# Optimization experiments

Hardware: AMD Instinct MI355X
Metric: run time of the kernel (lower is better)

## Reference

```python
import jax, jax.numpy as jnp
import numpy as np

N_NODES = 100000
N_EDGES = 3200000
N_GRAPHS = 128
IN_DIM = 4
HID = 64
BN_EPS = 1e-5


def setup_inputs() -> dict:
    key = jax.random.key(0)
    ks = jax.random.split(key, 24)
    x = jax.random.normal(ks[0], (N_NODES, IN_DIM), dtype=jnp.float32)
    edge_index = jax.random.randint(ks[1], (2, N_EDGES), 0, N_NODES, dtype=jnp.int32)
    batch_ids = jnp.sort(jax.random.randint(ks[2], (N_NODES,), 0, N_GRAPHS, dtype=jnp.int32))

    def lin(k, out_d, in_d):
        s = 1.0 / np.sqrt(in_d)
        return jax.random.uniform(k, (out_d, in_d), jnp.float32, -s, s)

    inp = {
        'x': x, 'edge_index': edge_index, 'batch_ids': batch_ids,
        # SAGEConv i: out = lin_l(mean_neighbors) + lin_r(x_self); bias lives in lin_l
        'w1l': lin(ks[3], HID, IN_DIM), 'b1': jnp.zeros((HID,), jnp.float32), 'w1r': lin(ks[4], HID, IN_DIM),
        'bn1_g': jnp.ones((HID,), jnp.float32), 'bn1_b': jnp.zeros((HID,), jnp.float32),
        'w2l': lin(ks[5], HID, HID), 'b2': jnp.zeros((HID,), jnp.float32), 'w2r': lin(ks[6], HID, HID),
        'bn2_g': jnp.ones((HID,), jnp.float32), 'bn2_b': jnp.zeros((HID,), jnp.float32),
        'w3l': lin(ks[7], HID, HID), 'b3': jnp.zeros((HID,), jnp.float32), 'w3r': lin(ks[8], HID, HID),
        'bn3_g': jnp.ones((HID,), jnp.float32), 'bn3_b': jnp.zeros((HID,), jnp.float32),
        'fc1_w': lin(ks[9], 64, HID), 'fc1_b': jnp.zeros((64,), jnp.float32),
        'fc2_w': lin(ks[10], 2, 64), 'fc2_b': jnp.zeros((2,), jnp.float32),
    }
    return inp


def _sage(x, src, dst, deg_inv, wl, bl, wr):
    # mean-aggregate neighbor messages (source -> target), then two small GEMMs
    msum = jax.ops.segment_sum(x[src], dst, num_segments=N_NODES)  # [N, d]
    agg = msum * deg_inv[:, None]
    return agg @ wl.T + bl + x @ wr.T


def _bn(x, g, b):
    # BatchNorm1d in training mode: batch stats over node dim, biased variance
    m = jnp.mean(x, axis=0)
    v = jnp.mean((x - m) ** 2, axis=0)
    return (x - m) * jax.lax.rsqrt(v + BN_EPS) * g + b


def reference(x, edge_index, batch_ids,
              w1l, b1, w1r, bn1_g, bn1_b,
              w2l, b2, w2r, bn2_g, bn2_b,
              w3l, b3, w3r, bn3_g, bn3_b,
              fc1_w, fc1_b, fc2_w, fc2_b):
    src, dst = edge_index[0], edge_index[1]
    deg = jax.ops.segment_sum(jnp.ones((src.shape[0],), x.dtype), dst, num_segments=N_NODES)
    deg_inv = 1.0 / jnp.maximum(deg, 1.0)

    h = jax.nn.relu(_bn(_sage(x, src, dst, deg_inv, w1l, b1, w1r), bn1_g, bn1_b))
    h = jax.nn.relu(_bn(_sage(h, src, dst, deg_inv, w2l, b2, w2r), bn2_g, bn2_b))
    h = jax.nn.relu(_bn(_sage(h, src, dst, deg_inv, w3l, b3, w3r), bn3_g, bn3_b))

    # global_mean_pool over graphs
    gsum = jax.ops.segment_sum(h, batch_ids, num_segments=N_GRAPHS)
    gcnt = jax.ops.segment_sum(jnp.ones((h.shape[0],), h.dtype), batch_ids, num_segments=N_GRAPHS)
    pooled = gsum / jnp.maximum(gcnt, 1.0)[:, None]

    # MLP head (dropout = identity at inference)
    hid = jax.nn.relu(pooled @ fc1_w.T + fc1_b)
    return hid @ fc2_w.T + fc2_b
```

## Files before the change

kernel.cpp:

```cpp
#include <hip/hip_runtime.h>
#include <hip/hip_fp16.h>

#define NN 100000
#define NE 3200000
#define NG 128
#define BN_EPS 1e-5f

#define NBUK 782
#define BSHIFT 7
#define BCAP 6144

#define GRID_SG 1024
#define PBMAX 2048
#define PSLICE 8

typedef _Float16 h2v __attribute__((ext_vector_type(2)));
typedef unsigned int u32x2 __attribute__((ext_vector_type(2)));
typedef unsigned int u32x4 __attribute__((ext_vector_type(4)));

static __device__ __forceinline__ h2v as_h2(unsigned int u) {
    return __builtin_bit_cast(h2v, u);
}
static __device__ __forceinline__ unsigned int as_u32(h2v h) {
    return __builtin_bit_cast(unsigned int, h);
}


__global__ void __launch_bounds__(512) k_scatter(
    const int* __restrict__ src, const int* __restrict__ dst,
    int* __restrict__ slab_cursor, unsigned int* __restrict__ slab, int E) {
    __shared__ int hist[NBUK + 2];
    __shared__ int cbase[NBUK + 2];
    int tid = threadIdx.x;
    int eBeg = blockIdx.x * 12500;
    int eEnd = min(eBeg + 12500, E);

    for (int t = tid; t < NBUK; t += 512) hist[t] = 0;
    __syncthreads();
    for (int e = eBeg + tid; e < eEnd; e += 512) {
        int b = dst[e] >> BSHIFT;
        atomicAdd(&hist[b], 1);
    }
    __syncthreads();
    for (int t = tid; t < NBUK; t += 512) {
        int c = hist[t];
        cbase[t] = (c > 0) ? atomicAdd(&slab_cursor[t], c) : 0;
    }
    __syncthreads();
    for (int t = tid; t < NBUK; t += 512) hist[t] = 0;
    __syncthreads();
    for (int e = eBeg + tid; e < eEnd; e += 512) {
        int d = dst[e];
        int b = d >> BSHIFT;
        int r = atomicAdd(&hist[b], 1);
        int pos = cbase[b] + r;
        if (pos < BCAP) slab[(size_t)b * BCAP + pos] = ((unsigned)src[e] << BSHIFT) | (unsigned)(d & 127);
    }
}

__global__ void __launch_bounds__(512) k_bucket_csr(
    const unsigned int* __restrict__ slab, const int* __restrict__ slab_cursor,
    int* __restrict__ row_ptr,
    float* __restrict__ deg_inv, int* __restrict__ csr_src,
    const float* __restrict__ x, const float* __restrict__ w1l,
    const float* __restrict__ b1, const float* __restrict__ w1r,
    __half* __restrict__ hp16, float* __restrict__ part) {
    __shared__ int lds_csr[BCAP];
    __shared__ int red[512];
    __shared__ int sdeg[128];
    __shared__ int sscan[128];
    __shared__ int slcur[128];
    __shared__ float swl[256], swr[256], sb1[64];
    __shared__ float ssum[64], ssq[64];
    int tid = threadIdx.x;
    int b = blockIdx.x;
    int lo = b << BSHIFT;
    int cnt = min(slab_cursor[b], BCAP);
    const unsigned int* sl = slab + (size_t)b * BCAP;

    int partial = 0;
    for (int j = tid; j < b; j += 512) partial += min(slab_cursor[j], BCAP);
    red[tid] = partial;
    __syncthreads();
    for (int off = 256; off > 0; off >>= 1) {
        if (tid < off) red[tid] += red[tid + off];
        __syncthreads();
    }
    int base = red[0];
    if (b == NBUK - 1 && tid == 0) row_ptr[NN] = base + cnt;

    if (tid < 256) { swl[tid] = w1l[tid]; swr[tid] = w1r[tid]; }
    if (tid < 64)  { sb1[tid] = b1[tid]; ssum[tid] = 0.f; ssq[tid] = 0.f; }
    if (tid < 128) sdeg[tid] = 0;
    __syncthreads();

    unsigned int myv[12];
    int mycount = 0;
    for (int k = tid; k < cnt; k += 512) myv[mycount++] = sl[k];
#pragma unroll
    for (int j = 0; j < 12; j++)
        if (j < mycount) atomicAdd(&sdeg[myv[j] & 127], 1);
    __syncthreads();
    int v = (tid < 128) ? sdeg[tid] : 0;
    if (tid < 128) sscan[tid] = v;
    __syncthreads();
    for (int off = 1; off < 128; off <<= 1) {
        int add = 0;
        if (tid < 128 && tid >= off) add = sscan[tid - off];
        __syncthreads();
        if (tid < 128) sscan[tid] += add;
        __syncthreads();
    }
    if (tid < 128) {
        int excl = sscan[tid] - v;
        int n = lo + tid;
        if (n < NN) {
            row_ptr[n] = base + excl;
            deg_inv[n] = 1.0f / fmaxf((float)v, 1.0f);
        }
        slcur[tid] = excl;
    }
    __syncthreads();
#pragma unroll
    for (int j = 0; j < 12; j++)
        if (j < mycount) {
            unsigned int p = myv[j];
            int pos = atomicAdd(&slcur[p & 127], 1);
            lds_csr[pos] = (int)(p >> BSHIFT);
        }
    __syncthreads();
    for (int k = tid; k < cnt; k += 512) csr_src[base + k] = lds_csr[k];

    int i = tid >> 2, c = tid & 3;
    int n = lo + i;
    bool valid = (n < NN);
    int dhi = sscan[i];
    int dlo = dhi - sdeg[i];
    const float4* x4 = (const float4*)x;
    float4 acc = make_float4(0.f, 0.f, 0.f, 0.f);
    int k = dlo + c;
    for (; k + 12 < dhi; k += 16) {
        int s0 = lds_csr[k], s1 = lds_csr[k + 4], s2 = lds_csr[k + 8], s3 = lds_csr[k + 12];
        float4 v0 = x4[s0];
        float4 v1 = x4[s1];
        float4 v2 = x4[s2];
        float4 v3 = x4[s3];
        acc.x += v0.x + v1.x + v2.x + v3.x;
        acc.y += v0.y + v1.y + v2.y + v3.y;
        acc.z += v0.z + v1.z + v2.z + v3.z;
        acc.w += v0.w + v1.w + v2.w + v3.w;
    }
    for (; k < dhi; k += 4) {
        int s = lds_csr[k];
        float4 xv = x4[s];
        acc.x += xv.x; acc.y += xv.y; acc.z += xv.z; acc.w += xv.w;
    }
#pragma unroll
    for (int m = 1; m <= 2; m <<= 1) {
        acc.x += __shfl_xor(acc.x, m);
        acc.y += __shfl_xor(acc.y, m);
        acc.z += __shfl_xor(acc.z, m);
        acc.w += __shfl_xor(acc.w, m);
    }
    float dv = 1.0f / fmaxf((float)sdeg[i], 1.0f);
    float ax = acc.x * dv, ay = acc.y * dv, az = acc.z * dv, aw = acc.w * dv;
    float4 xs = valid ? x4[n] : make_float4(0.f, 0.f, 0.f, 0.f);

#pragma unroll
    for (int m4 = 0; m4 < 4; m4++) {
        float4 o = make_float4(0.f, 0.f, 0.f, 0.f);
        float* op = &o.x;
        if (valid) {
#pragma unroll
            for (int t = 0; t < 4; t++) {
                int j = c * 16 + m4 * 4 + t;
                float s = sb1[j];
                s += ax * swl[j * 4 + 0] + ay * swl[j * 4 + 1] + az * swl[j * 4 + 2] + aw * swl[j * 4 + 3];
                s += xs.x * swr[j * 4 + 0] + xs.y * swr[j * 4 + 1] + xs.z * swr[j * 4 + 2] + xs.w * swr[j * 4 + 3];
                op[t] = s;
            }
            h2v p0 = h2v{(_Float16)o.x, (_Float16)o.y};
            h2v p1 = h2v{(_Float16)o.z, (_Float16)o.w};
            u32x2 w;
            w.x = *(unsigned int*)&p0;
            w.y = *(unsigned int*)&p1;
            __builtin_nontemporal_store(w, (u32x2*)hp16 + (size_t)n * 16 + c * 4 + m4);
        }
        float4 q = make_float4(o.x * o.x, o.y * o.y, o.z * o.z, o.w * o.w);
#pragma unroll
        for (int m = 4; m <= 32; m <<= 1) {
            o.x += __shfl_xor(o.x, m); o.y += __shfl_xor(o.y, m);
            o.z += __shfl_xor(o.z, m); o.w += __shfl_xor(o.w, m);
            q.x += __shfl_xor(q.x, m); q.y += __shfl_xor(q.y, m);
            q.z += __shfl_xor(q.z, m); q.w += __shfl_xor(q.w, m);
        }
        if ((tid & 63) < 4) {
            int jb = c * 16 + m4 * 4;
            atomicAdd(&ssum[jb + 0], o.x); atomicAdd(&ssum[jb + 1], o.y);
            atomicAdd(&ssum[jb + 2], o.z); atomicAdd(&ssum[jb + 3], o.w);
            atomicAdd(&ssq[jb + 0], q.x);  atomicAdd(&ssq[jb + 1], q.y);
            atomicAdd(&ssq[jb + 2], q.z);  atomicAdd(&ssq[jb + 3], q.w);
        }
    }
    __syncthreads();
    if (tid < 64) {
        part[(2 * tid) * PBMAX + blockIdx.x]     = ssum[tid];
        part[(2 * tid + 1) * PBMAX + blockIdx.x] = ssq[tid];
    }
}

__global__ void __launch_bounds__(256) k_bnact(
    const __half* __restrict__ hp, const float* __restrict__ sbv,
    __half* __restrict__ ha) {
    __shared__ float s_sc[64], s_bi[64];
    int tid = threadIdx.x;
    if (tid < 64) { s_sc[tid] = sbv[tid]; s_bi[tid] = sbv[64 + tid]; }
    __syncthreads();
    int c = tid & 7;
    h2v sc[4], bi[4];
#pragma unroll
    for (int j = 0; j < 4; j++) {
        sc[j] = h2v{(_Float16)s_sc[8 * c + 2 * j], (_Float16)s_sc[8 * c + 2 * j + 1]};
        bi[j] = h2v{(_Float16)s_bi[8 * c + 2 * j], (_Float16)s_bi[8 * c + 2 * j + 1]};
    }
    h2v hz = h2v{(_Float16)0.f, (_Float16)0.f};
    const u32x4* in4 = (const u32x4*)hp;
    u32x4* out4 = (u32x4*)ha;
    const int total = NN * 8;
    for (int i = blockIdx.x * 256 + tid; i < total; i += gridDim.x * 256) {
        u32x4 v = in4[i];
#pragma unroll
        for (int j = 0; j < 4; j++) {
            h2v a = as_h2(v[j]);
            a = __builtin_elementwise_max(a * sc[j] + bi[j], hz);
            v[j] = as_u32(a);
        }
        out4[i] = v;
    }
}

__global__ void __launch_bounds__(512, 8) k_sage(
    const __half* __restrict__ h_act,
    const int* __restrict__ row_ptr,
    const int* __restrict__ csr_src, const float* __restrict__ deg_inv,
    const float* __restrict__ wl, const float* __restrict__ bl,
    const float* __restrict__ wr, __half* __restrict__ hp16,
    float* __restrict__ part, int* __restrict__ wctr) {
    __shared__ h2v wl2s[32][68];
    __shared__ h2v wr2s[32][68];
    __shared__ h2v tAh[32][36];
    __shared__ h2v tXh[32][36];
    __shared__ float ssum[64], ssq[64];
    __shared__ int stile;
    int tid = threadIdx.x;
    for (int idx = tid; idx < 2048; idx += 512) {
        int j = idx & 63, kk = idx >> 6;
        float2 l = ((const float2*)wl)[j * 32 + kk];
        float2 r = ((const float2*)wr)[j * 32 + kk];
        wl2s[kk][j] = h2v{(_Float16)l.x, (_Float16)l.y};
        wr2s[kk][j] = h2v{(_Float16)r.x, (_Float16)r.y};
    }
    if (tid < 64) { ssum[tid] = 0.f; ssq[tid] = 0.f; }
    __syncthreads();

    int g = tid & 15, ni = tid >> 4;
    unsigned g8 = (unsigned)(g << 3);
    h2v hz = h2v{(_Float16)0.f, (_Float16)0.f};
    const char* hb = (const char*)h_act;
    const int ntiles = NN / 32;
    float4 bo = ((const float4*)bl)[g];

    int tile = blockIdx.x;
    while (true) {
        int n = (tile << 5) + ni;
        int r0 = row_ptr[n], r1 = row_ptr[n + 1];
        float di = deg_inv[n];
        uint2 rsv = *(const uint2*)(hb + (((unsigned)n << 7) | g8));
        float ax = 0.f, ay = 0.f, az = 0.f, aw = 0.f;
        int e = r0;
        for (; e + 8 <= r1; e += 8) {
            int s0 = csr_src[e],     s1 = csr_src[e + 1], s2 = csr_src[e + 2], s3 = csr_src[e + 3];
            int s4 = csr_src[e + 4], s5 = csr_src[e + 5], s6 = csr_src[e + 6], s7 = csr_src[e + 7];
            uint2 v0 = *(const uint2*)(hb + (((unsigned)s0 << 7) | g8));
            uint2 v1 = *(const uint2*)(hb + (((unsigned)s1 << 7) | g8));
            uint2 v2 = *(const uint2*)(hb + (((unsigned)s2 << 7) | g8));
            uint2 v3 = *(const uint2*)(hb + (((unsigned)s3 << 7) | g8));
            uint2 v4 = *(const uint2*)(hb + (((unsigned)s4 << 7) | g8));
            uint2 v5 = *(const uint2*)(hb + (((unsigned)s5 << 7) | g8));
            uint2 v6 = *(const uint2*)(hb + (((unsigned)s6 << 7) | g8));
            uint2 v7 = *(const uint2*)(hb + (((unsigned)s7 << 7) | g8));
            h2v hacc0 = hz, hacc1 = hz;
            hacc0 += as_h2(v0.x); hacc1 += as_h2(v0.y);
            hacc0 += as_h2(v1.x); hacc1 += as_h2(v1.y);
            hacc0 += as_h2(v2.x); hacc1 += as_h2(v2.y);
            hacc0 += as_h2(v3.x); hacc1 += as_h2(v3.y);
            hacc0 += as_h2(v4.x); hacc1 += as_h2(v4.y);
            hacc0 += as_h2(v5.x); hacc1 += as_h2(v5.y);
            hacc0 += as_h2(v6.x); hacc1 += as_h2(v6.y);
            hacc0 += as_h2(v7.x); hacc1 += as_h2(v7.y);
            ax += (float)hacc0.x; ay += (float)hacc0.y;
            az += (float)hacc1.x; aw += (float)hacc1.y;
        }
        for (; e < r1; ++e) {
            int s = csr_src[e];
            uint2 vv = *(const uint2*)(hb + (((unsigned)s << 7) | g8));
            h2v a0 = as_h2(vv.x), a1 = as_h2(vv.y);
            ax += (float)a0.x; ay += (float)a0.y; az += (float)a1.x; aw += (float)a1.y;
        }
        ax *= di; ay *= di; az *= di; aw *= di;
        tAh[ni][2 * g]     = h2v{(_Float16)ax, (_Float16)ay};
        tAh[ni][2 * g + 1] = h2v{(_Float16)az, (_Float16)aw};
        tXh[ni][2 * g]     = as_h2(rsv.x);
        tXh[ni][2 * g + 1] = as_h2(rsv.y);
        __syncthreads();

        if (tid == 0) stile = GRID_SG + atomicAdd(wctr, 1);

        float4 o = bo;
#pragma unroll
        for (int kk = 0; kk < 32; kk += 4) {
            u32x4 av = *(const u32x4*)&tAh[ni][kk];
            u32x4 xv = *(const u32x4*)&tXh[ni][kk];
#pragma unroll
            for (int j = 0; j < 4; j++) {
                u32x4 wlv = *(const u32x4*)&wl2s[kk + j][4 * g];
                u32x4 wrv = *(const u32x4*)&wr2s[kk + j][4 * g];
                h2v a2 = as_h2(av[j]);
                h2v x2 = as_h2(xv[j]);
#if __has_builtin(__builtin_amdgcn_fdot2)
                o.x = __builtin_amdgcn_fdot2(a2, as_h2(wlv[0]), o.x, false);
                o.y = __builtin_amdgcn_fdot2(a2, as_h2(wlv[1]), o.y, false);
                o.z = __builtin_amdgcn_fdot2(a2, as_h2(wlv[2]), o.z, false);
                o.w = __builtin_amdgcn_fdot2(a2, as_h2(wlv[3]), o.w, false);
                o.x = __builtin_amdgcn_fdot2(x2, as_h2(wrv[0]), o.x, false);
                o.y = __builtin_amdgcn_fdot2(x2, as_h2(wrv[1]), o.y, false);
                o.z = __builtin_amdgcn_fdot2(x2, as_h2(wrv[2]), o.z, false);
                o.w = __builtin_amdgcn_fdot2(x2, as_h2(wrv[3]), o.w, false);
#else
                {
                    h2v l0 = as_h2(wlv[0]), l1 = as_h2(wlv[1]), l2 = as_h2(wlv[2]), l3 = as_h2(wlv[3]);
                    h2v q0 = as_h2(wrv[0]), q1 = as_h2(wrv[1]), q2 = as_h2(wrv[2]), q3 = as_h2(wrv[3]);
                    float b0 = (float)a2.x, b1 = (float)a2.y, x0 = (float)x2.x, x1 = (float)x2.y;
                    o.x += b0 * (float)l0.x + b1 * (float)l0.y + x0 * (float)q0.x + x1 * (float)q0.y;
                    o.y += b0 * (float)l1.x + b1 * (float)l1.y + x0 * (float)q1.x + x1 * (float)q1.y;
                    o.z += b0 * (float)l2.x + b1 * (float)l2.y + x0 * (float)q2.x + x1 * (float)q2.y;
                    o.w += b0 * (float)l3.x + b1 * (float)l3.y + x0 * (float)q3.x + x1 * (float)q3.y;
                }
#endif
            }
        }
        {
            h2v p0 = h2v{(_Float16)o.x, (_Float16)o.y};
            h2v p1 = h2v{(_Float16)o.z, (_Float16)o.w};
            u32x2 w;
            w.x = *(unsigned int*)&p0;
            w.y = *(unsigned int*)&p1;
            __builtin_nontemporal_store(w, (u32x2*)hp16 + (size_t)n * 16 + g);
        }

        float4 qv = make_float4(o.x * o.x, o.y * o.y, o.z * o.z, o.w * o.w);
#pragma unroll
        for (int m = 16; m <= 32; m <<= 1) {
            o.x += __shfl_xor(o.x, m); o.y += __shfl_xor(o.y, m);
            o.z += __shfl_xor(o.z, m); o.w += __shfl_xor(o.w, m);
            qv.x += __shfl_xor(qv.x, m); qv.y += __shfl_xor(qv.y, m);
            qv.z += __shfl_xor(qv.z, m); qv.w += __shfl_xor(qv.w, m);
        }
        if ((tid & 48) == 0) {
            atomicAdd(&ssum[4 * g + 0], o.x); atomicAdd(&ssum[4 * g + 1], o.y);
            atomicAdd(&ssum[4 * g + 2], o.z); atomicAdd(&ssum[4 * g + 3], o.w);
            atomicAdd(&ssq[4 * g + 0], qv.x);  atomicAdd(&ssq[4 * g + 1], qv.y);
            atomicAdd(&ssq[4 * g + 2], qv.z);  atomicAdd(&ssq[4 * g + 3], qv.w);
        }
        __syncthreads();
        tile = stile;
        if (tile >= ntiles) break;
    }
    if (tid < 64) {
        part[(2 * tid) * PBMAX + blockIdx.x]     = ssum[tid];
        part[(2 * tid + 1) * PBMAX + blockIdx.x] = ssq[tid];
    }
}

__global__ void k_reduce_sb(const float* __restrict__ part, int PB,
                            const float* __restrict__ gamma, const float* __restrict__ beta,
                            float* __restrict__ sbv, int N) {
    int c = blockIdx.x;
    float s = 0.f, q = 0.f;
    for (int b = threadIdx.x; b < PB; b += 256) {
        s += part[(2 * c) * PBMAX + b];
        q += part[(2 * c + 1) * PBMAX + b];
    }
    __shared__ float rs[256], rq[256];
    rs[threadIdx.x] = s;
    rq[threadIdx.x] = q;
    __syncthreads();
    for (int off = 128; off > 0; off >>= 1) {
        if (threadIdx.x < off) {
            rs[threadIdx.x] += rs[threadIdx.x + off];
            rq[threadIdx.x] += rq[threadIdx.x + off];
        }
        __syncthreads();
    }
    if (threadIdx.x == 0) {
        float m = rs[0] / (float)N;
        float var = rq[0] / (float)N - m * m;
        float sc = gamma[c] * rsqrtf(var + BN_EPS);
        sbv[c]      = sc;
        sbv[64 + c] = beta[c] - m * sc;
    }
}

__global__ void __launch_bounds__(256) k_pool_partial(
    const __half* __restrict__ hp16, const float* __restrict__ sbv,
    const int* __restrict__ batch, float* __restrict__ pooled_part, int N) {
    __shared__ float ssc[64], sbi[64];
    __shared__ float sm[256];
    if (threadIdx.x < 64) {
        ssc[threadIdx.x] = sbv[threadIdx.x];
        sbi[threadIdx.x] = sbv[64 + threadIdx.x];
    }
    __syncthreads();
    int gph = blockIdx.x >> 3;
    int slice = blockIdx.x & 7;
    int lo = 0, hi = N;
    while (lo < hi) { int mid = (lo + hi) >> 1; if (batch[mid] < gph) lo = mid + 1; else hi = mid; }
    int start = lo;
    hi = N;
    while (lo < hi) { int mid = (lo + hi) >> 1; if (batch[mid] < gph + 1) lo = mid + 1; else hi = mid; }
    int end = lo;

    int c = threadIdx.x & 63, w = threadIdx.x >> 6;
    float s = 0.f;
    for (int r = start + slice * 4 + w; r < end; r += 32)
        s += fmaxf(__half2float(hp16[(size_t)r * 64 + c]) * ssc[c] + sbi[c], 0.f);
    sm[threadIdx.x] = s;
    __syncthreads();
    if (threadIdx.x < 64) {
        float t = sm[c] + sm[64 + c] + sm[128 + c] + sm[192 + c];
        pooled_part[(size_t)(gph * PSLICE + slice) * 64 + c] = t;
    }
}

__global__ void __launch_bounds__(64) k_head(
    const float* __restrict__ pooled_part, const int* __restrict__ batch,
    const float* __restrict__ fc1w, const float* __restrict__ fc1b,
    const float* __restrict__ fc2w, const float* __restrict__ fc2b,
    float* __restrict__ out, int N) {
    __shared__ float pl[64], hid[64];
    int gph = blockIdx.x;
    int j = threadIdx.x;
    int lo = 0, hi = N;
    while (lo < hi) { int mid = (lo + hi) >> 1; if (batch[mid] < gph) lo = mid + 1; else hi = mid; }
    int start = lo;
    hi = N;
    while (lo < hi) { int mid = (lo + hi) >> 1; if (batch[mid] < gph + 1) lo = mid + 1; else hi = mid; }
    int cnt = lo - start;

    float t = 0.f;
#pragma unroll
    for (int s = 0; s < PSLICE; s++) t += pooled_part[(size_t)(gph * PSLICE + s) * 64 + j];
    pl[j] = t / fmaxf((float)cnt, 1.0f);
    __syncthreads();
    float v = fc1b[j];
    for (int k = 0; k < 64; k++) v += pl[k] * fc1w[j * 64 + k];
    hid[j] = fmaxf(v, 0.f);
    __syncthreads();
    if (j < 2) {
        float o = fc2b[j];
        for (int k = 0; k < 64; k++) o += hid[k] * fc2w[j * 64 + k];
        out[gph * 2 + j] = o;
    }
}

extern "C" void kernel_launch(void* const* d_in, const int* in_sizes, int n_in,
                              void* d_out, int out_size, void* d_ws, size_t ws_size,
                              hipStream_t stream) {
    const float* x    = (const float*)d_in[0];
    const int* ei     = (const int*)d_in[1];
    const int* batch  = (const int*)d_in[2];
    const float* w1l  = (const float*)d_in[3];
    const float* b1   = (const float*)d_in[4];
    const float* w1r  = (const float*)d_in[5];
    const float* bn1g = (const float*)d_in[6];
    const float* bn1b = (const float*)d_in[7];
    const float* w2l  = (const float*)d_in[8];
    const float* b2   = (const float*)d_in[9];
    const float* w2r  = (const float*)d_in[10];
    const float* bn2g = (const float*)d_in[11];
    const float* bn2b = (const float*)d_in[12];
    const float* w3l  = (const float*)d_in[13];
    const float* b3   = (const float*)d_in[14];
    const float* w3r  = (const float*)d_in[15];
    const float* bn3g = (const float*)d_in[16];
    const float* bn3b = (const float*)d_in[17];
    const float* fc1w = (const float*)d_in[18];
    const float* fc1b = (const float*)d_in[19];
    const float* fc2w = (const float*)d_in[20];
    const float* fc2b = (const float*)d_in[21];
    float* out = (float*)d_out;

    const int N = NN, E = NE;
    const int* srcp = ei;
    const int* dstp = ei + E;

    char* ws = (char*)d_ws;
    size_t off = 0;
    auto alloc = [&](size_t bytes) -> char* {
        char* p = ws + off;
        off += (bytes + 255) & ~(size_t)255;
        return p;
    };
    int* csr_src       = (int*)alloc(sizeof(int) * E);
    __half* hpA        = (__half*)alloc(sizeof(__half) * N * 64);
    __half* hpB        = (__half*)alloc(sizeof(__half) * N * 64);
    unsigned int* slab = (unsigned int*)alloc(sizeof(unsigned int) * (size_t)NBUK * BCAP);
    int* slab_cursor   = (int*)alloc(sizeof(int) * NBUK);
    int* wctr          = (int*)alloc(sizeof(int) * 2);
    int* row_ptr       = (int*)alloc(sizeof(int) * (N + 1));
    float* deg_inv     = (float*)alloc(sizeof(float) * N);
    float* part        = (float*)alloc(sizeof(float) * 128 * PBMAX);
    float* sbv         = (float*)alloc(sizeof(float) * 128);
    float* pooled_part = (float*)alloc(sizeof(float) * NG * PSLICE * 64);

    __half* hAct = (__half*)slab;

    hipMemsetAsync(slab_cursor, 0, ((sizeof(int) * NBUK + 255) & ~(size_t)255) + sizeof(int) * 2, stream);

    k_scatter<<<256, 512, 0, stream>>>(srcp, dstp, slab_cursor, slab, E);
    k_bucket_csr<<<NBUK, 512, 0, stream>>>(slab, slab_cursor, row_ptr, deg_inv,
                                           csr_src, x, w1l, b1, w1r, hpA, part);
    k_reduce_sb<<<64, 256, 0, stream>>>(part, NBUK, bn1g, bn1b, sbv, N);

    k_bnact<<<1024, 256, 0, stream>>>(hpA, sbv, hAct);
    k_sage<<<GRID_SG, 512, 0, stream>>>(hAct, row_ptr, csr_src, deg_inv,
                                        w2l, b2, w2r, hpB, part, wctr);
    k_reduce_sb<<<64, 256, 0, stream>>>(part, GRID_SG, bn2g, bn2b, sbv, N);

    k_bnact<<<1024, 256, 0, stream>>>(hpB, sbv, hAct);
    k_sage<<<GRID_SG, 512, 0, stream>>>(hAct, row_ptr, csr_src, deg_inv,
                                        w3l, b3, w3r, hpA, part, wctr + 1);
    k_reduce_sb<<<64, 256, 0, stream>>>(part, GRID_SG, bn3g, bn3b, sbv, N);

    k_pool_partial<<<NG * PSLICE, 256, 0, stream>>>(hpA, sbv, batch, pooled_part, N);
    k_head<<<NG, 64, 0, stream>>>(pooled_part, batch, fc1w, fc1b, fc2w, fc2b, out, N);
}
```

Measured before the change: 401.2 us.

## Widen scatter grid, cache dst in registers, pad cursors, unroll layer-1 gather

The edge-bucketing scatter now runs on 1024 blocks of 3125 edges instead of 256 blocks of 12500. Each thread keeps its dst values in registers so the second pass does not reload them. Global bucket cursors are padded 16 ints apart, so concurrent atomics from different blocks land on separate cache lines. The layer-1 neighbour gather gets an 8-way unrolled loop to keep more loads in flight, at the cost of more global atomics on cursors and higher register use.

```diff
diff --git a/kernel.cpp b/kernel.cpp
--- a/kernel.cpp
+++ b/kernel.cpp
@@ -9,6 +9,10 @@
 #define NBUK 782
 #define BSHIFT 7
 #define BCAP 6144
+#define CURPAD 16
+
+#define SC_GRID 1024
+#define SC_EPB 3125
 
 #define GRID_SG 1024
 #define PBMAX 2048
@@ -32,29 +36,34 @@
     __shared__ int hist[NBUK + 2];
     __shared__ int cbase[NBUK + 2];
     int tid = threadIdx.x;
-    int eBeg = blockIdx.x * 12500;
-    int eEnd = min(eBeg + 12500, E);
+    int eBeg = blockIdx.x * SC_EPB;
+    int eEnd = min(eBeg + SC_EPB, E);
 
     for (int t = tid; t < NBUK; t += 512) hist[t] = 0;
     __syncthreads();
-    for (int e = eBeg + tid; e < eEnd; e += 512) {
-        int b = dst[e] >> BSHIFT;
-        atomicAdd(&hist[b], 1);
-    }
+    int myd[7];
+    int mc = 0;
+    for (int e = eBeg + tid; e < eEnd; e += 512) myd[mc++] = dst[e];
+#pragma unroll
+    for (int j = 0; j < 7; j++)
+        if (j < mc) atomicAdd(&hist[myd[j] >> BSHIFT], 1);
     __syncthreads();
     for (int t = tid; t < NBUK; t += 512) {
         int c = hist[t];
-        cbase[t] = (c > 0) ? atomicAdd(&slab_cursor[t], c) : 0;
+        cbase[t] = (c > 0) ? atomicAdd(&slab_cursor[t * CURPAD], c) : 0;
     }
     __syncthreads();
     for (int t = tid; t < NBUK; t += 512) hist[t] = 0;
     __syncthreads();
-    for (int e = eBeg + tid; e < eEnd; e += 512) {
-        int d = dst[e];
-        int b = d >> BSHIFT;
-        int r = atomicAdd(&hist[b], 1);
-        int pos = cbase[b] + r;
-        if (pos < BCAP) slab[(size_t)b * BCAP + pos] = ((unsigned)src[e] << BSHIFT) | (unsigned)(d & 127);
+    {
+        int i = 0;
+        for (int e = eBeg + tid; e < eEnd; e += 512, i++) {
+            int d = myd[i];
+            int b = d >> BSHIFT;
+            int r = atomicAdd(&hist[b], 1);
+            int pos = cbase[b] + r;
+            if (pos < BCAP) slab[(size_t)b * BCAP + pos] = ((unsigned)src[e] << BSHIFT) | (unsigned)(d & 127);
+        }
     }
 }
 
@@ -75,11 +84,11 @@
     int tid = threadIdx.x;
     int b = blockIdx.x;
     int lo = b << BSHIFT;
-    int cnt = min(slab_cursor[b], BCAP);
+    int cnt = min(slab_cursor[b * CURPAD], BCAP);
     const unsigned int* sl = slab + (size_t)b * BCAP;
 
     int partial = 0;
-    for (int j = tid; j < b; j += 512) partial += min(slab_cursor[j], BCAP);
+    for (int j = tid; j < b; j += 512) partial += min(slab_cursor[j * CURPAD], BCAP);
     red[tid] = partial;
     __syncthreads();
     for (int off = 256; off > 0; off >>= 1) {
@@ -139,6 +148,22 @@
     const float4* x4 = (const float4*)x;
     float4 acc = make_float4(0.f, 0.f, 0.f, 0.f);
     int k = dlo + c;
+    for (; k + 28 < dhi; k += 32) {
+        int s0 = lds_csr[k],      s1 = lds_csr[k + 4],  s2 = lds_csr[k + 8],  s3 = lds_csr[k + 12];
+        int s4 = lds_csr[k + 16], s5 = lds_csr[k + 20], s6 = lds_csr[k + 24], s7 = lds_csr[k + 28];
+        float4 v0 = x4[s0];
+        float4 v1 = x4[s1];
+        float4 v2 = x4[s2];
+        float4 v3 = x4[s3];
+        float4 v4 = x4[s4];
+        float4 v5 = x4[s5];
+        float4 v6 = x4[s6];
+        float4 v7 = x4[s7];
+        acc.x += v0.x + v1.x + v2.x + v3.x + v4.x + v5.x + v6.x + v7.x;
+        acc.y += v0.y + v1.y + v2.y + v3.y + v4.y + v5.y + v6.y + v7.y;
+        acc.z += v0.z + v1.z + v2.z + v3.z + v4.z + v5.z + v6.z + v7.z;
+        acc.w += v0.w + v1.w + v2.w + v3.w + v4.w + v5.w + v6.w + v7.w;
+    }
     for (; k + 12 < dhi; k += 16) {
         int s0 = lds_csr[k], s1 = lds_csr[k + 4], s2 = lds_csr[k + 8], s3 = lds_csr[k + 12];
         float4 v0 = x4[s0];
@@ -515,7 +540,7 @@
     __half* hpA        = (__half*)alloc(sizeof(__half) * N * 64);
     __half* hpB        = (__half*)alloc(sizeof(__half) * N * 64);
     unsigned int* slab = (unsigned int*)alloc(sizeof(unsigned int) * (size_t)NBUK * BCAP);
-    int* slab_cursor   = (int*)alloc(sizeof(int) * NBUK);
+    int* slab_cursor   = (int*)alloc(sizeof(int) * NBUK * CURPAD);
     int* wctr          = (int*)alloc(sizeof(int) * 2);
     int* row_ptr       = (int*)alloc(sizeof(int) * (N + 1));
     float* deg_inv     = (float*)alloc(sizeof(float) * N);
@@ -525,9 +550,10 @@
 
     __half* hAct = (__half*)slab;
 
-    hipMemsetAsync(slab_cursor, 0, ((sizeof(int) * NBUK + 255) & ~(size_t)255) + sizeof(int) * 2, stream);
-
-    k_scatter<<<256, 512, 0, stream>>>(srcp, dstp, slab_cursor, slab, E);
+    hipMemsetAsync(slab_cursor, 0,
+                   ((sizeof(int) * NBUK * CURPAD + 255) & ~(size_t)255) + sizeof(int) * 2, stream);
+
+    k_scatter<<<SC_GRID, 512, 0, stream>>>(srcp, dstp, slab_cursor, slab, E);
     k_bucket_csr<<<NBUK, 512, 0, stream>>>(slab, slab_cursor, row_ptr, deg_inv,
                                            csr_src, x, w1l, b1, w1r, hpA, part);
     k_reduce_sb<<<64, 256, 0, stream>>>(part, NBUK, bn1g, bn1b, sbv, N);
```

After: 426.9 us. 6.4% more time.
